# Kernel optimization log

Hardware: AMD Instinct MI355X
Metric: run time of the kernel (lower is better)

The kernel has to match this reference:

```python
import jax, jax.numpy as jnp
import numpy as np
from jax import lax

N = 20000        # nodes
E = 320000       # directed edges (avg degree 16)
F_IN = 512       # input feature dim
HID = 64         # hidden_layer
K_NEI = 8        # sampled neighbors per node
L = K_NEI + 1    # local subgraph size (self + neighbors)
N_TPL = 10       # N_templates
NT = 8           # N_templates_nodes
N_CLS = 6
ALPHA = 0.5      # FGW trade-off
EPS = 0.1        # entropic regularization
N_OUTER = 3      # outer CG iterations
N_SINK = 5       # sinkhorn iterations per outer step


def setup_inputs() -> dict:
    rng = np.random.default_rng(0)
    src = rng.integers(0, N, E).astype(np.int64)
    dst = rng.integers(0, N, E).astype(np.int64)
    edge_index = np.stack([src, dst])

    # fixed-size neighbor table (pad with self, mask)
    nbr = np.full((N, K_NEI), -1, np.int64)
    cnt = np.zeros(N, np.int64)
    for s, d in zip(src, dst):
        c = cnt[s]
        if c < K_NEI:
            nbr[s, c] = d
            cnt[s] = c + 1
    pad = nbr < 0
    self_col = np.arange(N, dtype=np.int64)
    nbr = np.where(pad, self_col[:, None], nbr)
    nbr_mask = np.concatenate([np.ones((N, 1)), (~pad).astype(np.float64)], 1).astype(np.float32)

    # local adjacency among {self, neighbors}: [N, L, L]
    idx_full = np.concatenate([self_col[:, None], nbr], 1)  # [N, L]
    edge_keys = np.unique(src * N + dst)
    keys = idx_full[:, :, None] * N + idx_full[:, None, :]
    C_local = np.isin(keys, edge_keys).astype(np.float32)

    ks = jax.random.split(jax.random.key(0), 10)
    x = jax.random.normal(ks[0], (N, F_IN), jnp.float32)
    W1 = jax.random.normal(ks[1], (F_IN, HID), jnp.float32) / np.float32(np.sqrt(F_IN))
    b1 = jnp.zeros((HID,), jnp.float32)
    W2 = jax.random.normal(ks[2], (HID, HID), jnp.float32) / np.float32(np.sqrt(HID))
    b2 = jnp.zeros((HID,), jnp.float32)
    t = jax.random.uniform(ks[3], (N_TPL, NT, NT), jnp.float32)
    templates = 0.5 * (t + jnp.swapaxes(t, 1, 2))  # symmetric template adjacency
    templates_features = jax.random.normal(ks[4], (N_TPL, NT, HID), jnp.float32)
    Wlin = jax.random.normal(ks[5], (HID + N_TPL, N_CLS), jnp.float32) / np.float32(np.sqrt(HID + N_TPL))
    blin = jnp.zeros((N_CLS,), jnp.float32)
    return {"x": x, "edge_index": jnp.asarray(edge_index), "nbr_idx": jnp.asarray(nbr),
            "nbr_mask": jnp.asarray(nbr_mask), "C_local": jnp.asarray(C_local),
            "W1": W1, "b1": b1, "W2": W2, "b2": b2,
            "templates": templates, "templates_features": templates_features,
            "Wlin": Wlin, "blin": blin}


def gcn(x, W, b, src, dst, n):
    xw = x @ W
    sl = jnp.arange(n)
    s = jnp.concatenate([src, sl])
    d = jnp.concatenate([dst, sl])
    deg = jax.ops.segment_sum(jnp.ones_like(s, jnp.float32), d, num_segments=n)
    dinv = lax.rsqrt(deg)
    coef = dinv[s] * dinv[d]
    return jax.ops.segment_sum(xw[s] * coef[:, None], d, num_segments=n) + b


def fgw_dist(M, C1, h1, C2, h2):
    # entropic fused GW (square loss) with fixed iterations; padded rows have h1 = 0
    f1 = C1 * C1
    f2 = C2 * C2
    constC = (f1 @ h1)[:, None] + (f2 @ h2)[None, :]
    T0 = h1[:, None] * h2[None, :]

    def outer(T, _):
        tens = constC - 2.0 * (C1 @ T @ C2)
        G = (1.0 - ALPHA) * M + ALPHA * tens
        Kmat = jnp.exp(-G / EPS)

        def sink(carry, _):
            u, v = carry
            u = h1 / (Kmat @ v + 1e-16)
            v = h2 / (Kmat.T @ u + 1e-16)
            return (u, v), None

        (u, v), _ = lax.scan(sink, (jnp.ones_like(h1), jnp.ones_like(h2)), None, length=N_SINK)
        return u[:, None] * Kmat * v[None, :], None

    T, _ = lax.scan(outer, T0, None, length=N_OUTER)
    tens = constC - 2.0 * (C1 @ T @ C2)
    return jnp.sum(T * ((1.0 - ALPHA) * M + ALPHA * tens))


def distance_to_template(x, nbr_idx, nbr_mask, C_local, templates_features, templates):
    n = x.shape[0]
    idx_full = jnp.concatenate([jnp.arange(n)[:, None], nbr_idx], axis=1)  # [N, L]
    xl = x[idx_full]  # [N, L, HID]
    # squared euclidean cost to each template: [N, T, L, NT]
    inner = jnp.einsum('nld,tmd->ntlm', xl, templates_features)
    M = (jnp.sum(xl * xl, -1)[:, None, :, None]
         + jnp.sum(templates_features * templates_features, -1)[None, :, None, :]
         - 2.0 * inner)
    h1 = nbr_mask / jnp.sum(nbr_mask, -1, keepdims=True)  # [N, L]
    h2 = jnp.full((NT,), 1.0 / NT, jnp.float32)

    per_tpl = jax.vmap(fgw_dist, in_axes=(0, None, None, 0, None))
    per_node = jax.vmap(per_tpl, in_axes=(0, 0, 0, None, None))
    return per_node(M, C_local, h1, templates, h2)  # [N, N_TPL]


def reference(x, edge_index, nbr_idx, nbr_mask, C_local, W1, b1, W2, b2,
              templates, templates_features, Wlin, blin):
    src, dst = edge_index[0], edge_index[1]
    n = x.shape[0]
    h = jax.nn.relu(gcn(x, W1, b1, src, dst, n))
    h = gcn(h, W2, b2, src, dst, n)
    y = distance_to_template(h, nbr_idx, nbr_mask, C_local, templates_features, templates)
    out = jnp.concatenate([h, y], axis=1) @ Wlin + blin
    return jax.nn.relu(out)
```

## Files before the change

kernel.cpp:

```cpp
#include <hip/hip_runtime.h>


#define NN   20000
#define EE   320000
#define FIN  512
#define HID  64
#define KNEI 8
#define LSZ  9
#define NTPL 10
#define NTN  8
#define NCLS 6
#define CAP  48

typedef unsigned short bf16_t;
typedef unsigned short us8 __attribute__((ext_vector_type(8)));

__device__ __forceinline__ float b2f(bf16_t u) {
  union { unsigned int i; float f; } v; v.i = ((unsigned int)u) << 16; return v.f;
}
__device__ __forceinline__ bf16_t f2b(float f) {
  union { float f; unsigned int i; } v; v.f = f;
  unsigned int x = v.i;
  return (bf16_t)((x + 0x7fffu + ((x >> 16) & 1u)) >> 16);
}
__device__ __forceinline__ float ldf(const void* p, long i, int fp32) {
  return fp32 ? ((const float*)p)[i] : b2f(((const bf16_t*)p)[i]);
}
__device__ __forceinline__ int ldi(const void* p, long i, int i64) {
  return i64 ? (int)((const long long*)p)[i] : ((const int*)p)[i];
}
__device__ __forceinline__ float frcp(float x) { return __builtin_amdgcn_rcpf(x); }

__global__ __launch_bounds__(256) void probe_kernel(const void* __restrict__ x,
                                                    const void* __restrict__ ei,
                                                    const void* __restrict__ tfeat,
                                                    int* __restrict__ flags,
                                                    float* __restrict__ tn2min,
                                                    int* __restrict__ pos) {
  int tid = threadIdx.x;
  int zi = blockIdx.x * 256 + tid;
  if (zi < NN) pos[zi] = 0;
  if (blockIdx.x != 0) return;

  __shared__ int sfl[2];
  __shared__ float tn2s[80];
  if (tid == 0) {
    int sane = 0;
    for (int k = 0; k < 64; k += 2) {
      bf16_t u = ((const bf16_t*)x)[k];
      int e = (u >> 7) & 0xff;
      if (e >= 112 && e <= 142) sane++;
    }
    int f0 = (sane < 24) ? 1 : 0;
    int zc = 0;
    for (int k = 1; k < 64; k += 2)
      if (((const int*)ei)[k] == 0) zc++;
    int f1 = (zc >= 16) ? 1 : 0;
    flags[0] = f0; flags[1] = f1;
    sfl[0] = f0; sfl[1] = f1;
  }
  __syncthreads();
  if (tid < 80) {
    int fF = sfl[0];
    float s = 0.f;
    for (int k = 0; k < HID; ++k) {
      float v = ldf(tfeat, (long)tid * HID + k, fF);
      s += v * v;
    }
    tn2s[tid] = s;
  }
  __syncthreads();
  if (tid == 0) {
    float gmin = 1e30f;
    for (int t = 0; t < NTPL; ++t) {
      float m = tn2s[t * 8];
      for (int r = 1; r < 8; ++r) m = fminf(m, tn2s[t * 8 + r]);
      tn2min[t] = m;
      gmin = fminf(gmin, m);
    }
    tn2min[NTPL] = gmin;
  }
}

__global__ __launch_bounds__(256) void scatter_kernel(const void* __restrict__ ei,
                                                      int* __restrict__ pos,
                                                      int* __restrict__ slot,
                                                      const int* __restrict__ flags) {
  int i = blockIdx.x * 256 + threadIdx.x;
  if (i >= EE) return;
  int i64 = flags[1];
  int s = ldi(ei, i, i64);
  int d = ldi(ei, (long)EE + i, i64);
  int p = atomicAdd(&pos[d], 1);
  if (p < CAP) slot[d * CAP + p] = s;
}

__global__ __launch_bounds__(256) void gemm1_kernel(const void* __restrict__ x,
                                                    const void* __restrict__ W1,
                                                    const int* __restrict__ cnt,
                                                    float* __restrict__ xw1,
                                                    const int* __restrict__ flags) {
  int wave = blockIdx.x * 4 + (threadIdx.x >> 6);
  int lane = threadIdx.x & 63;
  int row0 = wave * 4;
  if (row0 >= NN) return;
  float a0 = 0.f, a1 = 0.f, a2 = 0.f, a3 = 0.f;
  if (!flags[0]) {
    const bf16_t* xb = (const bf16_t*)x + (long)row0 * FIN;
    const bf16_t* wp = (const bf16_t*)W1;
#pragma unroll 2
    for (int k8 = 0; k8 < FIN / 8; ++k8) {
      us8 r0 = *(const us8*)(xb + k8 * 8);
      us8 r1 = *(const us8*)(xb + FIN + k8 * 8);
      us8 r2 = *(const us8*)(xb + 2 * FIN + k8 * 8);
      us8 r3 = *(const us8*)(xb + 3 * FIN + k8 * 8);
#pragma unroll
      for (int q = 0; q < 8; ++q) {
        float w = b2f(wp[(k8 * 8 + q) * HID + lane]);
        a0 += b2f(r0[q]) * w;
        a1 += b2f(r1[q]) * w;
        a2 += b2f(r2[q]) * w;
        a3 += b2f(r3[q]) * w;
      }
    }
  } else {
    const float* x0 = (const float*)x + (long)row0 * FIN;
    const float* wp = (const float*)W1;
#pragma unroll 8
    for (int k = 0; k < FIN; ++k) {
      float w = wp[k * HID + lane];
      a0 += x0[k] * w;
      a1 += x0[FIN + k] * w;
      a2 += x0[2 * FIN + k] * w;
      a3 += x0[3 * FIN + k] * w;
    }
  }
  float d0 = rsqrtf((float)cnt[row0 + 0] + 1.0f);
  float d1 = rsqrtf((float)cnt[row0 + 1] + 1.0f);
  float d2 = rsqrtf((float)cnt[row0 + 2] + 1.0f);
  float d3 = rsqrtf((float)cnt[row0 + 3] + 1.0f);
  xw1[(long)(row0 + 0) * HID + lane] = a0 * d0;
  xw1[(long)(row0 + 1) * HID + lane] = a1 * d1;
  xw1[(long)(row0 + 2) * HID + lane] = a2 * d2;
  xw1[(long)(row0 + 3) * HID + lane] = a3 * d3;
}

__global__ __launch_bounds__(256) void gatherA_kernel(const float* __restrict__ sxw,
                                                      const int* __restrict__ cnt,
                                                      const int* __restrict__ slot,
                                                      float* __restrict__ sxw2,
                                                      const void* __restrict__ b1v,
                                                      const void* __restrict__ W2,
                                                      const int* __restrict__ flags) {
  int n = blockIdx.x * 4 + (threadIdx.x >> 6);
  if (n >= NN) return;
  int fF = flags[0];
  int c = threadIdx.x & 63;
  float acc = sxw[(long)n * HID + c];
  int m = cnt[n]; if (m > CAP) m = CAP;
  const int* sl = slot + (long)n * CAP;
  float accB = 0.f;
  for (int e0 = 0; e0 < m; e0 += 8) {
    int4 sa = *(const int4*)(sl + e0);
    int4 sb = *(const int4*)(sl + e0 + 4);
    if (e0 + 0 < m) acc  += sxw[(long)sa.x * HID + c];
    if (e0 + 1 < m) accB += sxw[(long)sa.y * HID + c];
    if (e0 + 2 < m) acc  += sxw[(long)sa.z * HID + c];
    if (e0 + 3 < m) accB += sxw[(long)sa.w * HID + c];
    if (e0 + 4 < m) acc  += sxw[(long)sb.x * HID + c];
    if (e0 + 5 < m) accB += sxw[(long)sb.y * HID + c];
    if (e0 + 6 < m) acc  += sxw[(long)sb.z * HID + c];
    if (e0 + 7 < m) accB += sxw[(long)sb.w * HID + c];
  }
  float dn = rsqrtf((float)cnt[n] + 1.0f);
  float h1 = (acc + accB) * dn + ldf(b1v, c, fF);
  h1 = h1 > 0.f ? h1 : 0.f;

  float o = 0.f;
#pragma unroll 8
  for (int k = 0; k < HID; ++k)
    o += __shfl(h1, k) * ldf(W2, k * HID + c, fF);
  sxw2[(long)n * HID + c] = o * dn;
}

__global__ __launch_bounds__(256) void gatherB_kernel(const float* __restrict__ sxw,
                                                      const int* __restrict__ cnt,
                                                      const int* __restrict__ slot,
                                                      float* __restrict__ h,
                                                      float* __restrict__ n2,
                                                      const void* __restrict__ b2v,
                                                      const int* __restrict__ flags) {
  int n = blockIdx.x * 4 + (threadIdx.x >> 6);
  if (n >= NN) return;
  int c = threadIdx.x & 63;
  float acc = sxw[(long)n * HID + c];
  int m = cnt[n]; if (m > CAP) m = CAP;
  const int* sl = slot + (long)n * CAP;
  float accB = 0.f;
  for (int e0 = 0; e0 < m; e0 += 8) {
    int4 sa = *(const int4*)(sl + e0);
    int4 sb = *(const int4*)(sl + e0 + 4);
    if (e0 + 0 < m) acc  += sxw[(long)sa.x * HID + c];
    if (e0 + 1 < m) accB += sxw[(long)sa.y * HID + c];
    if (e0 + 2 < m) acc  += sxw[(long)sa.z * HID + c];
    if (e0 + 3 < m) accB += sxw[(long)sa.w * HID + c];
    if (e0 + 4 < m) acc  += sxw[(long)sb.x * HID + c];
    if (e0 + 5 < m) accB += sxw[(long)sb.y * HID + c];
    if (e0 + 6 < m) acc  += sxw[(long)sb.z * HID + c];
    if (e0 + 7 < m) accB += sxw[(long)sb.w * HID + c];
  }
  float dn = rsqrtf((float)cnt[n] + 1.0f);
  float h2 = (acc + accB) * dn;
  h[(long)n * HID + c] = h2;
  float v = h2 + ldf(b2v, c, flags[0]);
  float s = v * v;
  s += __shfl_xor(s, 1); s += __shfl_xor(s, 2); s += __shfl_xor(s, 4);
  s += __shfl_xor(s, 8); s += __shfl_xor(s, 16); s += __shfl_xor(s, 32);
  if (c == 0) n2[n] = s;
}

#define NODES_PB 4
#define TPN 80
#define XLP 65

__global__ __launch_bounds__(320, 2) void fgw_kernel(
    const float* __restrict__ h2,
    const void* __restrict__ b2v,
    const void* __restrict__ nbr_idx,
    const void* __restrict__ nbr_mask,
    const void* __restrict__ C_local,
    const void* __restrict__ tmpl,
    const void* __restrict__ tfeat,
    const void* __restrict__ Wlin,
    const void* __restrict__ blin,
    void* __restrict__ out,
    const int* __restrict__ flags,
    const float* __restrict__ tn2min,
    const float* __restrict__ n2)
{
  const int tid = threadIdx.x;
  const int fF = flags[0];
  const int fI = flags[1];
  const int nb = tid / TPN;
  const int local = tid - nb * TPN;
  const int t = local >> 3;
  const int j = local & 7;
  const int n = blockIdx.x * NODES_PB + nb;
  const int lane = tid & 63;
  const int ob = lane & 56;

  __shared__ float xlS[NODES_PB][LSZ][XLP];
  __shared__ float C1S[NODES_PB][81];
  __shared__ float hwS[NODES_PB][LSZ];
  __shared__ float f1S[NODES_PB][LSZ];
  __shared__ float xnS[NODES_PB][LSZ];
  __shared__ float distS[NODES_PB][NTPL];
  __shared__ float xmaxS[NODES_PB];
  __shared__ int   needS[NODES_PB];
  __shared__ int   sidxS[NODES_PB][LSZ];
  __shared__ float WlinS[(HID + NTPL) * NCLS + NCLS];

  for (int i = tid; i < (HID + NTPL) * NCLS; i += 320)
    WlinS[i] = ldf(Wlin, i, fF);
  if (tid < NCLS) WlinS[(HID + NTPL) * NCLS + tid] = ldf(blin, tid, fF);

  if (local < LSZ) {
    int idx = (local == 0) ? n : ldi(nbr_idx, (long)n * KNEI + local - 1, fI);
    sidxS[nb][local] = idx;
    xnS[nb][local] = n2[idx];
  }
  if (local < HID)
    xlS[nb][0][local] = h2[(long)n * HID + local] + ldf(b2v, local, fF);
  __syncthreads();

  if (local == 0) {
    float xm = xnS[nb][0];
#pragma unroll
    for (int l = 1; l < LSZ; ++l) xm = fmaxf(xm, xnS[nb][l]);
    xmaxS[nb] = xm;
    needS[nb] = ((sqrtf(tn2min[NTPL]) - sqrtf(xm)) >= 5.0990195f) ? 0 : 1;
  }
  __syncthreads();

  const int need = needS[nb];
  if (need) {
    for (int i = local; i < 8 * HID; i += TPN) {
      int l = 1 + (i >> 6), k = i & 63;
      xlS[nb][l][k] = h2[(long)sidxS[nb][l] * HID + k] + ldf(b2v, k, fF);
    }
    for (int i = local; i < 81; i += TPN)
      C1S[nb][i] = ldf(C_local, (long)n * 81 + i, fF);
  }
  __syncthreads();

  if (need && local < LSZ) {
    int l = local;
    float msum = 0.f, f1 = 0.f;
#pragma unroll
    for (int jj = 0; jj < LSZ; ++jj) {
      float mj = ldf(nbr_mask, (long)n * LSZ + jj, fF);
      msum += mj;
      float c = C1S[nb][l * LSZ + jj];
      f1 += c * c * mj;
    }
    float inv = frcp(msum);
    hwS[nb][l] = ldf(nbr_mask, (long)n * LSZ + l, fF) * inv;
    f1S[nb][l] = f1 * inv;
  }
  __syncthreads();

  bool slow = need && ((sqrtf(tn2min[t]) - sqrtf(xmaxS[nb])) < 5.0990195f);
  if (slow) {
    float C2c[NTN];
    float f2h2;
    {
      float s = 0.f;
#pragma unroll
      for (int m = 0; m < NTN; ++m) {
        C2c[m] = ldf(tmpl, t * 64 + m * 8 + j, fF);
        float r = ldf(tmpl, t * 64 + j * 8 + m, fF);
        s += r * r;
      }
      f2h2 = s * 0.125f;
    }
    float hwr[LSZ], f1r[LSZ];
#pragma unroll
    for (int l = 0; l < LSZ; ++l) { hwr[l] = hwS[nb][l]; f1r[l] = f1S[nb][l]; }

    float Mc[LSZ];
    {
      float accI[LSZ];
#pragma unroll
      for (int l = 0; l < LSZ; ++l) accI[l] = 0.f;
      float tn2 = 0.f;
      const long tb = (long)local * HID;
      for (int kb = 0; kb < 8; ++kb) {
        float r[8];
#pragma unroll
        for (int q = 0; q < 8; ++q) r[q] = ldf(tfeat, tb + kb * 8 + q, fF);
#pragma unroll
        for (int q = 0; q < 8; ++q) tn2 += r[q] * r[q];
#pragma unroll
        for (int l = 0; l < LSZ; ++l) {
          float s = 0.f;
#pragma unroll
          for (int q = 0; q < 8; ++q) s += xlS[nb][l][kb * 8 + q] * r[q];
          accI[l] += s;
        }
      }
#pragma unroll
      for (int l = 0; l < LSZ; ++l)
        Mc[l] = xnS[nb][l] + tn2 - 2.f * accI[l];
    }

    float Tc[LSZ], Kc[LSZ], u[LSZ];
#pragma unroll
    for (int l = 0; l < LSZ; ++l) Tc[l] = hwr[l] * 0.125f;

    float v = 1.0f;
    for (int outer = 0; outer < 3; ++outer) {
      float Ac[LSZ];
#pragma unroll
      for (int l = 0; l < LSZ; ++l) {
        float s = 0.f;
#pragma unroll
        for (int l2 = 0; l2 < LSZ; ++l2) s += C1S[nb][l * LSZ + l2] * Tc[l2];
        Ac[l] = s;
      }
#pragma unroll
      for (int l = 0; l < LSZ; ++l) {
        float s = 0.f;
#pragma unroll
        for (int m = 0; m < NTN; ++m) s += __shfl(Ac[l], ob + m) * C2c[m];
        float tens = f1r[l] + f2h2 - 2.f * s;
        Kc[l] = __expf(-5.0f * (Mc[l] + tens));
      }
      v = 1.0f;
      for (int it = 0; it < 5; ++it) {
#pragma unroll
        for (int l = 0; l < LSZ; ++l) {
          float p = Kc[l] * v;
          p += __shfl_xor(p, 1); p += __shfl_xor(p, 2); p += __shfl_xor(p, 4);
          u[l] = hwr[l] * frcp(p + 1e-16f);
        }
        float s = 0.f;
#pragma unroll
        for (int l = 0; l < LSZ; ++l) s += Kc[l] * u[l];
        v = 0.125f * frcp(s + 1e-16f);
      }
#pragma unroll
      for (int l = 0; l < LSZ; ++l) Tc[l] = u[l] * Kc[l] * v;
    }
    {
      float Ac[LSZ];
#pragma unroll
      for (int l = 0; l < LSZ; ++l) {
        float s = 0.f;
#pragma unroll
        for (int l2 = 0; l2 < LSZ; ++l2) s += C1S[nb][l * LSZ + l2] * Tc[l2];
        Ac[l] = s;
      }
      float cl = 0.f;
#pragma unroll
      for (int l = 0; l < LSZ; ++l) {
        float s = 0.f;
#pragma unroll
        for (int m = 0; m < NTN; ++m) s += __shfl(Ac[l], ob + m) * C2c[m];
        float tens = f1r[l] + f2h2 - 2.f * s;
        cl += Tc[l] * 0.5f * (Mc[l] + tens);
      }
      cl += __shfl_xor(cl, 1); cl += __shfl_xor(cl, 2); cl += __shfl_xor(cl, 4);
      if (j == 0) distS[nb][t] = cl;
    }
  } else if (j == 0) {
    distS[nb][t] = 0.f;
  }
  __syncthreads();

  if (local < NCLS) {
    int c = local;
    float acc = WlinS[(HID + NTPL) * NCLS + c];
#pragma unroll
    for (int k = 0; k < HID; ++k)
      acc += xlS[nb][0][k] * WlinS[k * NCLS + c];
#pragma unroll
    for (int tt = 0; tt < NTPL; ++tt)
      acc += distS[nb][tt] * WlinS[(HID + tt) * NCLS + c];
    float r = acc > 0.f ? acc : 0.f;
    if (fF) ((float*)out)[(long)n * NCLS + c] = r;
    else    ((bf16_t*)out)[(long)n * NCLS + c] = f2b(r);
  }
}

extern "C" void kernel_launch(void* const* d_in, const int* in_sizes, int n_in,
                              void* d_out, int out_size, void* d_ws, size_t ws_size,
                              hipStream_t stream) {
  (void)n_in; (void)out_size;
  const void* x     = d_in[0];
  const void* ei    = d_in[1];
  const void* nbr   = d_in[2];
  const void* nmask = d_in[3];
  const void* Cl    = d_in[4];
  const void* W1    = d_in[5];
  const void* b1    = d_in[6];
  const void* W2    = d_in[7];
  const void* b2    = d_in[8];
  const void* tmpl  = d_in[9];
  const void* tfeat = d_in[10];
  const void* Wlin  = d_in[11];
  const void* blin  = d_in[12];

  int*    flags  = (int*)d_ws;
  float*  tn2min = (float*)d_ws + 4;
  float*  n2     = (float*)d_ws + 16;
  int*    pos    = (int*)(n2 + NN);
  int*    slot   = pos + NN;
  float*  bufA   = (float*)(slot + (long)CAP * NN);
  float*  bufB   = bufA + (long)NN * HID;
  void*   xc     = (void*)(bufB + (long)NN * HID);
  const size_t BASE_BYTES = (size_t)(16 + 2 * NN + (long)CAP * NN
                                     + 2 * (long)NN * HID) * 4;

  const void* xsrc = x;
  if (in_sizes) {
    size_t s0 = (size_t)(unsigned)in_sizes[0];
    if ((s0 == (size_t)NN * FIN * 2 || s0 == (size_t)NN * FIN * 4) &&
        ws_size >= BASE_BYTES + s0) {
      hipMemcpyAsync(xc, x, s0, hipMemcpyDeviceToDevice, stream);
      xsrc = xc;
    }
  }

  probe_kernel<<<79, 256, 0, stream>>>(x, ei, tfeat, flags, tn2min, pos);
  scatter_kernel<<<(EE + 255) / 256, 256, 0, stream>>>(ei, pos, slot, flags);

  gemm1_kernel<<<NN / 16, 256, 0, stream>>>(xsrc, W1, pos, bufA, flags);
  gatherA_kernel<<<NN / 4, 256, 0, stream>>>(bufA, pos, slot, bufB, b1, W2, flags);
  gatherB_kernel<<<NN / 4, 256, 0, stream>>>(bufB, pos, slot, bufA, n2, b2, flags);

  fgw_kernel<<<NN / NODES_PB, 320, 0, stream>>>(bufA, b2, nbr, nmask, Cl, tmpl,
                                                tfeat, Wlin, blin, d_out, flags,
                                                tn2min, n2);
}
```

Baseline: 314.0 us.

## Drop x device copy, store neighbor slots as uint16, split gemm1 launches

Removes the device-to-device copy of the input feature matrix into workspace and reads x directly in gemm1. Shrinks the CSR-like slot table from 32-bit to 16-bit indices, which halves the index traffic in both gather kernels and loads eight indices per vector read. It also splits gemm1 into five row-slice launches, which adds launch overhead. The 16-bit indices are only valid because N=20000 is below 65536.

After: 328.9 us. 1.05x slower.

```diff
diff --git a/kernel.cpp b/kernel.cpp
--- a/kernel.cpp
+++ b/kernel.cpp
@@ -11,6 +11,7 @@
 #define NTN  8
 #define NCLS 6
 #define CAP  48
+#define GSLICE 4000
 
 typedef unsigned short bf16_t;
 typedef unsigned short us8 __attribute__((ext_vector_type(8)));
@@ -84,7 +85,7 @@
 
 __global__ __launch_bounds__(256) void scatter_kernel(const void* __restrict__ ei,
                                                       int* __restrict__ pos,
-                                                      int* __restrict__ slot,
+                                                      unsigned short* __restrict__ slot,
                                                       const int* __restrict__ flags) {
   int i = blockIdx.x * 256 + threadIdx.x;
   if (i >= EE) return;
@@ -92,18 +93,21 @@
   int s = ldi(ei, i, i64);
   int d = ldi(ei, (long)EE + i, i64);
   int p = atomicAdd(&pos[d], 1);
-  if (p < CAP) slot[d * CAP + p] = s;
+  if (p < CAP) slot[(long)d * CAP + p] = (unsigned short)s;
 }
 
 __global__ __launch_bounds__(256) void gemm1_kernel(const void* __restrict__ x,
                                                     const void* __restrict__ W1,
                                                     const int* __restrict__ cnt,
                                                     float* __restrict__ xw1,
-                                                    const int* __restrict__ flags) {
+                                                    const int* __restrict__ flags,
+                                                    int rowbase) {
   int wave = blockIdx.x * 4 + (threadIdx.x >> 6);
   int lane = threadIdx.x & 63;
-  int row0 = wave * 4;
-  if (row0 >= NN) return;
+  int row0 = rowbase + wave * 4;
+  if (row0 + 3 >= NN) {
+    if (row0 >= NN) return;
+  }
   float a0 = 0.f, a1 = 0.f, a2 = 0.f, a3 = 0.f;
   if (!flags[0]) {
     const bf16_t* xb = (const bf16_t*)x + (long)row0 * FIN;
@@ -147,7 +151,7 @@
 
 __global__ __launch_bounds__(256) void gatherA_kernel(const float* __restrict__ sxw,
                                                       const int* __restrict__ cnt,
-                                                      const int* __restrict__ slot,
+                                                      const unsigned short* __restrict__ slot,
                                                       float* __restrict__ sxw2,
                                                       const void* __restrict__ b1v,
                                                       const void* __restrict__ W2,
@@ -158,19 +162,18 @@
   int c = threadIdx.x & 63;
   float acc = sxw[(long)n * HID + c];
   int m = cnt[n]; if (m > CAP) m = CAP;
-  const int* sl = slot + (long)n * CAP;
+  const unsigned short* sl = slot + (long)n * CAP;
   float accB = 0.f;
   for (int e0 = 0; e0 < m; e0 += 8) {
-    int4 sa = *(const int4*)(sl + e0);
-    int4 sb = *(const int4*)(sl + e0 + 4);
-    if (e0 + 0 < m) acc  += sxw[(long)sa.x * HID + c];
-    if (e0 + 1 < m) accB += sxw[(long)sa.y * HID + c];
-    if (e0 + 2 < m) acc  += sxw[(long)sa.z * HID + c];
-    if (e0 + 3 < m) accB += sxw[(long)sa.w * HID + c];
-    if (e0 + 4 < m) acc  += sxw[(long)sb.x * HID + c];
-    if (e0 + 5 < m) accB += sxw[(long)sb.y * HID + c];
-    if (e0 + 6 < m) acc  += sxw[(long)sb.z * HID + c];
-    if (e0 + 7 < m) accB += sxw[(long)sb.w * HID + c];
+    us8 s8 = *(const us8*)(sl + e0);
+    if (e0 + 0 < m) acc  += sxw[(long)s8[0] * HID + c];
+    if (e0 + 1 < m) accB += sxw[(long)s8[1] * HID + c];
+    if (e0 + 2 < m) acc  += sxw[(long)s8[2] * HID + c];
+    if (e0 + 3 < m) accB += sxw[(long)s8[3] * HID + c];
+    if (e0 + 4 < m) acc  += sxw[(long)s8[4] * HID + c];
+    if (e0 + 5 < m) accB += sxw[(long)s8[5] * HID + c];
+    if (e0 + 6 < m) acc  += sxw[(long)s8[6] * HID + c];
+    if (e0 + 7 < m) accB += sxw[(long)s8[7] * HID + c];
   }
   float dn = rsqrtf((float)cnt[n] + 1.0f);
   float h1 = (acc + accB) * dn + ldf(b1v, c, fF);
@@ -185,7 +188,7 @@
 
 __global__ __launch_bounds__(256) void gatherB_kernel(const float* __restrict__ sxw,
                                                       const int* __restrict__ cnt,
-                                                      const int* __restrict__ slot,
+                                                      const unsigned short* __restrict__ slot,
                                                       float* __restrict__ h,
                                                       float* __restrict__ n2,
                                                       const void* __restrict__ b2v,
@@ -195,19 +198,18 @@
   int c = threadIdx.x & 63;
   float acc = sxw[(long)n * HID + c];
   int m = cnt[n]; if (m > CAP) m = CAP;
-  const int* sl = slot + (long)n * CAP;
+  const unsigned short* sl = slot + (long)n * CAP;
   float accB = 0.f;
   for (int e0 = 0; e0 < m; e0 += 8) {
-    int4 sa = *(const int4*)(sl + e0);
-    int4 sb = *(const int4*)(sl + e0 + 4);
-    if (e0 + 0 < m) acc  += sxw[(long)sa.x * HID + c];
-    if (e0 + 1 < m) accB += sxw[(long)sa.y * HID + c];
-    if (e0 + 2 < m) acc  += sxw[(long)sa.z * HID + c];
-    if (e0 + 3 < m) accB += sxw[(long)sa.w * HID + c];
-    if (e0 + 4 < m) acc  += sxw[(long)sb.x * HID + c];
-    if (e0 + 5 < m) accB += sxw[(long)sb.y * HID + c];
-    if (e0 + 6 < m) acc  += sxw[(long)sb.z * HID + c];
-    if (e0 + 7 < m) accB += sxw[(long)sb.w * HID + c];
+    us8 s8 = *(const us8*)(sl + e0);
+    if (e0 + 0 < m) acc  += sxw[(long)s8[0] * HID + c];
+    if (e0 + 1 < m) accB += sxw[(long)s8[1] * HID + c];
+    if (e0 + 2 < m) acc  += sxw[(long)s8[2] * HID + c];
+    if (e0 + 3 < m) accB += sxw[(long)s8[3] * HID + c];
+    if (e0 + 4 < m) acc  += sxw[(long)s8[4] * HID + c];
+    if (e0 + 5 < m) accB += sxw[(long)s8[5] * HID + c];
+    if (e0 + 6 < m) acc  += sxw[(long)s8[6] * HID + c];
+    if (e0 + 7 < m) accB += sxw[(long)s8[7] * HID + c];
   }
   float dn = rsqrtf((float)cnt[n] + 1.0f);
   float h2 = (acc + accB) * dn;
@@ -435,7 +437,7 @@
 extern "C" void kernel_launch(void* const* d_in, const int* in_sizes, int n_in,
                               void* d_out, int out_size, void* d_ws, size_t ws_size,
                               hipStream_t stream) {
-  (void)n_in; (void)out_size;
+  (void)in_sizes; (void)n_in; (void)out_size; (void)ws_size;
   const void* x     = d_in[0];
   const void* ei    = d_in[1];
   const void* nbr   = d_in[2];
@@ -450,31 +452,20 @@
   const void* Wlin  = d_in[11];
   const void* blin  = d_in[12];
 
-  int*    flags  = (int*)d_ws;
-  float*  tn2min = (float*)d_ws + 4;
-  float*  n2     = (float*)d_ws + 16;
-  int*    pos    = (int*)(n2 + NN);
-  int*    slot   = pos + NN;
-  float*  bufA   = (float*)(slot + (long)CAP * NN);
-  float*  bufB   = bufA + (long)NN * HID;
-  void*   xc     = (void*)(bufB + (long)NN * HID);
-  const size_t BASE_BYTES = (size_t)(16 + 2 * NN + (long)CAP * NN
-                                     + 2 * (long)NN * HID) * 4;
-
-  const void* xsrc = x;
-  if (in_sizes) {
-    size_t s0 = (size_t)(unsigned)in_sizes[0];
-    if ((s0 == (size_t)NN * FIN * 2 || s0 == (size_t)NN * FIN * 4) &&
-        ws_size >= BASE_BYTES + s0) {
-      hipMemcpyAsync(xc, x, s0, hipMemcpyDeviceToDevice, stream);
-      xsrc = xc;
-    }
-  }
+  int*            flags  = (int*)d_ws;
+  float*          tn2min = (float*)d_ws + 4;
+  float*          n2     = (float*)d_ws + 16;
+  int*            pos    = (int*)(n2 + NN);
+  unsigned short* slot   = (unsigned short*)(pos + NN);
+  float*          bufA   = (float*)((int*)(pos + NN) + (long)CAP * NN / 2);
+  float*          bufB   = bufA + (long)NN * HID;
 
   probe_kernel<<<79, 256, 0, stream>>>(x, ei, tfeat, flags, tn2min, pos);
   scatter_kernel<<<(EE + 255) / 256, 256, 0, stream>>>(ei, pos, slot, flags);
 
-  gemm1_kernel<<<NN / 16, 256, 0, stream>>>(xsrc, W1, pos, bufA, flags);
+  for (int s = 0; s < 5; ++s)
+    gemm1_kernel<<<GSLICE / 16, 256, 0, stream>>>(x, W1, pos, bufA, flags,
+                                                  s * GSLICE);
   gatherA_kernel<<<NN / 4, 256, 0, stream>>>(bufA, pos, slot, bufB, b1, W2, flags);
   gatherB_kernel<<<NN / 4, 256, 0, stream>>>(bufB, pos, slot, bufA, n2, b2, flags);
 
```
